# Kernel optimization log

Measured on AMD Instinct MI355X. Metric: run time of the kernel, lower is better.

The kernel has to match this reference:

```python
import jax, jax.numpy as jnp
import numpy as np


def setup_inputs() -> dict:
    key = jax.random.key(0)
    k1, k2 = jax.random.split(key)
    B, L, D = 8, 2048, 256
    x = jax.random.normal(k1, (B, L, D), dtype=jnp.float32)
    x_mask = jax.random.randint(k2, (B, L), 0, 2).astype(bool)  # True = padded key position
    return {"x": x, "x_mask": x_mask}


def reference(x, x_mask):
    # x: [B, L, D], x_mask: [B, L] bool (True = masked/padding)
    B, L, D = x.shape
    # Unscaled self-attention scores: [B, L, L]
    scores = jnp.einsum('bld,bmd->blm', x, x)
    # Diagonal exclusion: score of token with itself set to 0 (not -inf!)
    eye = jnp.eye(L, dtype=bool)
    scores = jnp.where(eye[None, :, :], jnp.float32(0.0), scores)
    # Padding mask: mask key columns with -inf (applied after diagonal zeroing,
    # so a masked diagonal entry ends up -inf, matching the torch order of ops)
    scores = jnp.where(x_mask[:, None, :], -jnp.inf, scores)
    a = jax.nn.softmax(scores, axis=2)
    return jnp.einsum('blm,bmd->bld', a, x)
```

## Files before the change

kernel.cpp:

```cpp
#include <hip/hip_runtime.h>
#include <hip/hip_bf16.h>

#define B_ 8
#define L_ 2048
#define D_ 256
#define BK 32
#define KSPLIT 2
#define KQ (L_/KSPLIT)
#define NIT (KQ/BK)
#define PSTR 40
#define NROW (B_*L_)
#define NE ((size_t)B_*L_*D_)
#define THR 13.0f
#define MINIT (-1e30f)
#define LOG2E_F 1.44269504f

typedef __attribute__((ext_vector_type(8))) _Float16 f16x8;
typedef __attribute__((ext_vector_type(4))) _Float16 hf4;
typedef __attribute__((ext_vector_type(4))) float f32x4;

#define MFMA16F(a,b,c) __builtin_amdgcn_mfma_f32_16x16x32_f16((a),(b),(c),0,0,0)
#define NEG_INF (-__builtin_inff())
#define GLL(src,dst) __builtin_amdgcn_global_load_lds( \
    (const __attribute__((address_space(1))) void*)(src), \
    (__attribute__((address_space(3))) void*)(dst), 16, 0, 0)

__device__ __forceinline__ f32x4 fmax4(f32x4 a, f32x4 b){
  f32x4 r;
  r[0]=fmaxf(a[0],b[0]); r[1]=fmaxf(a[1],b[1]);
  r[2]=fmaxf(a[2],b[2]); r[3]=fmaxf(a[3],b[3]);
  return r;
}

__global__ void prep_k(const float* __restrict__ x,
                       _Float16* __restrict__ x16,
                       _Float16* __restrict__ vtl){
  __shared__ _Float16 T[32][258];
  const int t = threadIdx.x;
  const int tIdx = blockIdx.x;
  const int b = blockIdx.y;
  const int l0 = tIdx*32;

  #pragma unroll
  for (int i=0;i<4;++i){
    const int n8 = t + 256*i;
    const int row = n8>>5;
    const int c   = (n8&31)*8;
    size_t idx = ((size_t)(b*L_ + l0 + row))*D_ + c;
    float4 v0 = *(const float4*)(x + idx);
    float4 v1 = *(const float4*)(x + idx + 4);
    f16x8 h;
    h[0]=(_Float16)v0.x; h[1]=(_Float16)v0.y; h[2]=(_Float16)v0.z; h[3]=(_Float16)v0.w;
    h[4]=(_Float16)v1.x; h[5]=(_Float16)v1.y; h[6]=(_Float16)v1.z; h[7]=(_Float16)v1.w;
    *(f16x8*)(x16 + idx) = h;
    *(f16x8*)(&T[row][c]) = h;
  }
  __syncthreads();

  _Float16* vb = vtl + ((size_t)(b*64 + tIdx))*8192;
  #pragma unroll
  for (int i=0;i<4;++i){
    const int q = t + 256*i;
    const int d = q>>2, ph = q&3;
    const int kc = ph ^ ((d>>1)&3);
    const int k0 = kc*8;
    f16x8 h;
    #pragma unroll
    for (int j=0;j<8;++j) h[j] = T[k0+j][d];
    *(f16x8*)(vb + (size_t)q*8) = h;
  }
}

__launch_bounds__(256, 2)
__global__ void flash_k(const _Float16* __restrict__ x16,
                        const _Float16* __restrict__ vtl,
                        const int* __restrict__ mask,
                        _Float16* __restrict__ oall,
                        float* __restrict__ mll,
                        float* __restrict__ mm){
  __shared__ __attribute__((aligned(16))) _Float16 sK[2][8192];
  __shared__ __attribute__((aligned(16))) _Float16 sV[2][8192];
  __shared__ __attribute__((aligned(16))) _Float16 sP[2][4][16*PSTR];

  const int tid  = threadIdx.x;
  const int wave = tid >> 6, lane = tid & 63;
  const int quad = lane >> 4, l16 = lane & 15;
  const int b = blockIdx.y, z = blockIdx.z;
  const int q0w = blockIdx.x*64 + wave*16;
  const int sw = l16 & 7, vsw = (l16>>1)&3;

  f16x8 qh[8];
  {
    const _Float16* qr = x16 + ((size_t)(b*L_ + q0w + l16))*D_;
    const _Float16 l2e = (_Float16)LOG2E_F;
    #pragma unroll
    for (int ks=0; ks<8; ++ks){
      f16x8 h = *(const f16x8*)(qr + ks*32 + quad*8);
      #pragma unroll
      for (int j=0;j<8;++j) h[j] = h[j] * l2e;
      qh[ks] = h;
    }
  }
  unsigned long long mb = 0;
  {
    const int* mrow = mask + b*L_ + z*KQ;
    #pragma unroll
    for (int j=0;j<64;++j)
      mb |= (unsigned long long)(mrow[j*16 + l16] ? 1u : 0u) << j;
  }

  f32x4 M = (f32x4){MINIT, MINIT, MINIT, MINIT};

  unsigned kof[4], vof[4], dof[4];
  #pragma unroll
  for (int i=0;i<4;++i){
    int c = (wave + i*4)*64 + lane;
    int r = c>>5, pk = c&31;
    kof[i] = (unsigned)(r*512 + ((pk ^ (r&7))*16));
    vof[i] = (unsigned)(c*16);
    dof[i] = (unsigned)((wave + i*4)*1024);
  }
  const char* kbase = (const char*)x16 + ((size_t)b*L_ + (size_t)z*KQ)*(D_*2);
  const char* vbase = (const char*)vtl + ((size_t)(b*64 + z*32))*16384;

  #pragma unroll
  for (int i=0;i<4;++i) GLL(kbase + kof[i], (char*)sK[0] + dof[i]);

  f32x4 O[16], Osum;
  #pragma unroll
  for (int i=0;i<16;i++) O[i] = (f32x4){0.f,0.f,0.f,0.f};
  Osum = (f32x4){0.f,0.f,0.f,0.f};
  f16x8 ones;
  #pragma unroll
  for (int j=0;j<8;++j) ones[j] = (_Float16)1.0f;

  __syncthreads();

  for (int it=0; it<NIT; ++it){
    if (it+1 < NIT){
      const char* kb2 = kbase + (size_t)(it+1)*16384;
      char* kd = (char*)sK[(it+1)&1];
      #pragma unroll
      for (int i=0;i<4;++i) GLL(kb2 + kof[i], kd + dof[i]);
    }
    {
      const char* vb2 = vbase + (size_t)it*16384;
      char* vd = (char*)sV[it&1];
      #pragma unroll
      for (int i=0;i<4;++i) GLL(vb2 + vof[i], vd + dof[i]);
    }
    const _Float16* kb = sK[it&1];

    f32x4 S[2];
    S[0]=(f32x4){0,0,0,0}; S[1]=(f32x4){0,0,0,0};
    #pragma unroll
    for (int ks=0; ks<8; ++ks){
      f16x8 b0 = *(const f16x8*)(kb + (     l16)*256 + (((ks*4+quad)^sw)*8));
      f16x8 b1 = *(const f16x8*)(kb + (16 + l16)*256 + (((ks*4+quad)^sw)*8));
      S[0] = MFMA16F(qh[ks], b0, S[0]);
      S[1] = MFMA16F(qh[ks], b1, S[1]);
    }

    if (it > 0){
      const _Float16* vb = sV[(it-1)&1];
      f16x8 pf = *(const f16x8*)(&sP[(it-1)&1][wave][l16*PSTR + quad*8]);
      #pragma unroll
      for (int vt=0; vt<16; ++vt){
        f16x8 bv = *(const f16x8*)(vb + (vt*16+l16)*32 + ((quad^vsw)*8));
        O[vt] = MFMA16F(pf, bv, O[vt]);
      }
      Osum = MFMA16F(pf, ones, Osum);
    }

    {
      const int d0 = q0w - (z*KQ + it*BK);
      if ((unsigned)d0 < 32u){
        const int ntd = d0 >> 4;
        #pragma unroll
        for (int r=0;r<4;++r)
          S[ntd][r] = (l16 == quad*4+r) ? 0.0f : S[ntd][r];
      }
    }
    {
      const unsigned mw = (unsigned)(mb >> (unsigned)(it*2));
      const float mk0 = (mw & 1u) ? NEG_INF : 0.0f;
      const float mk1 = (mw & 2u) ? NEG_INF : 0.0f;
      #pragma unroll
      for (int r=0;r<4;++r){ S[0][r] += mk0; S[1][r] += mk1; }
    }

    {
      f32x4 t = fmax4(S[0], S[1]);
      int ok = 1;
      #pragma unroll
      for (int r=0;r<4;++r) ok &= (t[r] <= M[r] + THR);
      if (!__all(ok)){
        #pragma unroll
        for (int off=1; off<16; off<<=1){
          f32x4 o;
          o[0]=__shfl_xor(t[0],off); o[1]=__shfl_xor(t[1],off);
          o[2]=__shfl_xor(t[2],off); o[3]=__shfl_xor(t[3],off);
          t = fmax4(t,o);
        }
        f32x4 mn = fmax4(M, t);
        float sc[4];
        #pragma unroll
        for (int r=0;r<4;++r) sc[r] = exp2f(M[r] - mn[r]);
        #pragma unroll
        for (int vt=0; vt<16; ++vt){
          #pragma unroll
          for (int r=0;r<4;++r) O[vt][r] *= sc[r];
        }
        #pragma unroll
        for (int r=0;r<4;++r) Osum[r] *= sc[r];
        M = mn;
      }
    }

    #pragma unroll
    for (int r=0;r<4;++r){
      const int row = quad*4 + r;
      sP[it&1][wave][row*PSTR +      l16] = (_Float16)exp2f(S[0][r] - M[r]);
      sP[it&1][wave][row*PSTR + 16 + l16] = (_Float16)exp2f(S[1][r] - M[r]);
    }

    __syncthreads();
  }

  {
    const _Float16* vb = sV[(NIT-1)&1];
    f16x8 pf = *(const f16x8*)(&sP[(NIT-1)&1][wave][l16*PSTR + quad*8]);
    #pragma unroll
    for (int vt=0; vt<16; ++vt){
      f16x8 bv = *(const f16x8*)(vb + (vt*16+l16)*32 + ((quad^vsw)*8));
      O[vt] = MFMA16F(pf, bv, O[vt]);
    }
    Osum = MFMA16F(pf, ones, Osum);
  }

  {
    const int u = b*(L_/16) + blockIdx.x*4 + wave;
    _Float16* ob = oall + (size_t)z*NE + (size_t)u*4096;
    #pragma unroll
    for (int vt=0; vt<16; ++vt){
      hf4 hh;
      #pragma unroll
      for (int r=0;r<4;++r) hh[r] = (_Float16)O[vt][r];
      *(hf4*)(ob + vt*256 + lane*4) = hh;
    }
    if (l16 == 0){
      const int row = u*16 + quad*4;
      #pragma unroll
      for (int r=0;r<4;++r){
        mll[z*NROW + row + r] = Osum[r];
        mm [z*NROW + row + r] = M[r];
      }
    }
  }
}

__global__ void combine_k(float* __restrict__ out,
                          const _Float16* __restrict__ oall,
                          const float* __restrict__ mll,
                          const float* __restrict__ mm){
  __shared__ float T2[16][260];
  const int t = threadIdx.x, u = blockIdx.x;
  const int quad = (t>>4)&3, l16 = t&15;
  const int row0 = u*16 + quad*4;

  f32x4 mz[KSPLIT], lz[KSPLIT];
  #pragma unroll
  for (int zc=0; zc<KSPLIT; ++zc){
    mz[zc] = *(const f32x4*)(mm  + zc*NROW + row0);
    lz[zc] = *(const f32x4*)(mll + zc*NROW + row0);
  }
  f32x4 ms = mz[0];
  #pragma unroll
  for (int zc=1; zc<KSPLIT; ++zc) ms = fmax4(ms, mz[zc]);

  float sc[KSPLIT][4];
  f32x4 den = (f32x4){0.f,0.f,0.f,0.f};
  #pragma unroll
  for (int zc=0; zc<KSPLIT; ++zc){
    #pragma unroll
    for (int r=0;r<4;++r){
      sc[zc][r] = exp2f(mz[zc][r] - ms[r]);
      den[r] += sc[zc][r] * lz[zc][r];
    }
  }
  float inv[4];
  #pragma unroll
  for (int r=0;r<4;++r) inv[r] = 1.0f/den[r];

  #pragma unroll
  for (int i=0;i<4;++i){
    const int f = t + 256*i;
    const int vt = f>>6;
    float acc[4] = {0.f,0.f,0.f,0.f};
    #pragma unroll
    for (int zc=0; zc<KSPLIT; ++zc){
      hf4 v = *(const hf4*)(oall + (size_t)zc*NE + (size_t)u*4096 + (size_t)f*4);
      #pragma unroll
      for (int r=0;r<4;++r) acc[r] += sc[zc][r] * (float)v[r];
    }
    #pragma unroll
    for (int r=0;r<4;++r) T2[quad*4+r][vt*16+l16] = acc[r]*inv[r];
  }
  __syncthreads();
  #pragma unroll
  for (int p=0;p<4;++p){
    const int row = (t>>6) + p*4, col = (t&63)*4;
    float4 vv = *(const float4*)&T2[row][col];
    *(float4*)(out + ((size_t)u*16 + row)*D_ + col) = vv;
  }
}

extern "C" void kernel_launch(void* const* d_in, const int* in_sizes, int n_in,
                              void* d_out, int out_size, void* d_ws, size_t ws_size,
                              hipStream_t stream) {
  const float* x    = (const float*)d_in[0];
  const int*   mask = (const int*)d_in[1];
  float*       out  = (float*)d_out;

  _Float16* x16  = (_Float16*)d_ws;
  _Float16* vtl  = x16 + NE;
  _Float16* oall = vtl + NE;
  float*    mll  = (float*)(oall + (size_t)KSPLIT*NE);
  float*    mm   = mll + (size_t)KSPLIT*NROW;

  prep_k   <<<dim3(L_/32, B_), dim3(256), 0, stream>>>(x, x16, vtl);
  flash_k  <<<dim3(L_/64, B_, KSPLIT), dim3(256), 0, stream>>>(x16, vtl, mask, oall, mll, mm);
  combine_k<<<dim3(NROW/16), dim3(256), 0, stream>>>(out, oall, mll, mm);
}
```

Baseline: 148.4 us.

## Fuse prep, flash and combine into one cooperative kernel with grid syncs

Replaces the three launches with a single cooperative kernel of 512 blocks. Each block first does the fp16 conversion and V transpose, then runs a grid sync, then the split-K flash pass. After a second grid sync, the z=0 blocks merge the z=1 partial results straight from their registers. This removes two kernel launch gaps and the z=0 half of the partial-output round trip through global memory. In exchange it pays for two grid-wide barriers, and it needs all 512 blocks resident at two per CU, with a fallback to the old three-kernel path if the cooperative launch fails.

```diff
diff --git a/kernel.cpp b/kernel.cpp
--- a/kernel.cpp
+++ b/kernel.cpp
@@ -1,5 +1,7 @@
 #include <hip/hip_runtime.h>
-#include <hip/hip_bf16.h>
+#include <hip/hip_cooperative_groups.h>
+
+namespace cg = cooperative_groups;
 
 #define B_ 8
 #define L_ 2048
@@ -32,21 +34,18 @@
   return r;
 }
 
-__global__ void prep_k(const float* __restrict__ x,
-                       _Float16* __restrict__ x16,
-                       _Float16* __restrict__ vtl){
-  __shared__ _Float16 T[32][258];
-  const int t = threadIdx.x;
-  const int tIdx = blockIdx.x;
-  const int b = blockIdx.y;
+__device__ __forceinline__ void prep_core(const float* __restrict__ x,
+                                          _Float16* __restrict__ x16,
+                                          _Float16* __restrict__ vtl,
+                                          int tIdx, int bb, int t, char* smem){
+  _Float16 (*T)[258] = (_Float16(*)[258])smem;
   const int l0 = tIdx*32;
-
   #pragma unroll
   for (int i=0;i<4;++i){
     const int n8 = t + 256*i;
     const int row = n8>>5;
     const int c   = (n8&31)*8;
-    size_t idx = ((size_t)(b*L_ + l0 + row))*D_ + c;
+    size_t idx = ((size_t)(bb*L_ + l0 + row))*D_ + c;
     float4 v0 = *(const float4*)(x + idx);
     float4 v1 = *(const float4*)(x + idx + 4);
     f16x8 h;
@@ -56,8 +55,7 @@
     *(f16x8*)(&T[row][c]) = h;
   }
   __syncthreads();
-
-  _Float16* vb = vtl + ((size_t)(b*64 + tIdx))*8192;
+  _Float16* vb = vtl + ((size_t)(bb*64 + tIdx))*8192;
   #pragma unroll
   for (int i=0;i<4;++i){
     const int q = t + 256*i;
@@ -71,22 +69,19 @@
   }
 }
 
-__launch_bounds__(256, 2)
-__global__ void flash_k(const _Float16* __restrict__ x16,
-                        const _Float16* __restrict__ vtl,
-                        const int* __restrict__ mask,
-                        _Float16* __restrict__ oall,
-                        float* __restrict__ mll,
-                        float* __restrict__ mm){
-  __shared__ __attribute__((aligned(16))) _Float16 sK[2][8192];
-  __shared__ __attribute__((aligned(16))) _Float16 sV[2][8192];
-  __shared__ __attribute__((aligned(16))) _Float16 sP[2][4][16*PSTR];
-
-  const int tid  = threadIdx.x;
-  const int wave = tid >> 6, lane = tid & 63;
+__device__ __forceinline__ void flash_core(const _Float16* __restrict__ x16,
+                                           const _Float16* __restrict__ vtl,
+                                           const int* __restrict__ mask,
+                                           char* smem, int b, int z, int qblk,
+                                           int wave, int lane,
+                                           f32x4 (&O)[16], f32x4& Osum, f32x4& M){
+  _Float16 (*sK)[8192] = (_Float16(*)[8192])smem;
+  _Float16 (*sV)[8192] = (_Float16(*)[8192])(smem + 32768);
+  typedef _Float16 sPhalf[4][16*PSTR];
+  sPhalf* sP = (sPhalf*)(smem + 65536);
+
   const int quad = lane >> 4, l16 = lane & 15;
-  const int b = blockIdx.y, z = blockIdx.z;
-  const int q0w = blockIdx.x*64 + wave*16;
+  const int q0w = qblk*64 + wave*16;
   const int sw = l16 & 7, vsw = (l16>>1)&3;
 
   f16x8 qh[8];
@@ -109,7 +104,7 @@
       mb |= (unsigned long long)(mrow[j*16 + l16] ? 1u : 0u) << j;
   }
 
-  f32x4 M = (f32x4){MINIT, MINIT, MINIT, MINIT};
+  M = (f32x4){MINIT, MINIT, MINIT, MINIT};
 
   unsigned kof[4], vof[4], dof[4];
   #pragma unroll
@@ -126,7 +121,6 @@
   #pragma unroll
   for (int i=0;i<4;++i) GLL(kbase + kof[i], (char*)sK[0] + dof[i]);
 
-  f32x4 O[16], Osum;
   #pragma unroll
   for (int i=0;i<16;i++) O[i] = (f32x4){0.f,0.f,0.f,0.f};
   Osum = (f32x4){0.f,0.f,0.f,0.f};
@@ -237,10 +231,34 @@
     }
     Osum = MFMA16F(pf, ones, Osum);
   }
-
-  {
-    const int u = b*(L_/16) + blockIdx.x*4 + wave;
-    _Float16* ob = oall + (size_t)z*NE + (size_t)u*4096;
+}
+
+__launch_bounds__(256, 2)
+__global__ void fused_k(const float* __restrict__ x,
+                        const int* __restrict__ mask,
+                        float* __restrict__ out,
+                        _Float16* __restrict__ x16,
+                        _Float16* __restrict__ vtl,
+                        _Float16* __restrict__ oall,
+                        float* __restrict__ mll,
+                        float* __restrict__ mm){
+  __shared__ __attribute__((aligned(16))) char smem[75776];
+  const int tid = threadIdx.x;
+  const int bid = blockIdx.x;
+  const int wave = tid >> 6, lane = tid & 63;
+  const int quad = lane >> 4, l16 = lane & 15;
+
+  prep_core(x, x16, vtl, bid & 63, bid >> 6, tid, smem);
+  cg::this_grid().sync();
+
+  const int z = bid >> 8, b = (bid >> 5) & 7, qblk = bid & 31;
+  f32x4 O[16], Osum, M;
+  flash_core(x16, vtl, mask, smem, b, z, qblk, wave, lane, O, Osum, M);
+
+  const int u = b*(L_/16) + qblk*4 + wave;
+
+  if (z == 1){
+    _Float16* ob = oall + (size_t)u*4096;
     #pragma unroll
     for (int vt=0; vt<16; ++vt){
       hf4 hh;
@@ -252,17 +270,87 @@
       const int row = u*16 + quad*4;
       #pragma unroll
       for (int r=0;r<4;++r){
-        mll[z*NROW + row + r] = Osum[r];
-        mm [z*NROW + row + r] = M[r];
+        mll[row + r] = Osum[r];
+        mm [row + r] = M[r];
       }
     }
   }
-}
-
-__global__ void combine_k(float* __restrict__ out,
-                          const _Float16* __restrict__ oall,
-                          const float* __restrict__ mll,
-                          const float* __restrict__ mm){
+  cg::this_grid().sync();
+  if (z == 1) return;
+
+  const int row0 = u*16 + quad*4;
+  f32x4 mz1 = *(const f32x4*)(mm  + row0);
+  f32x4 lz1 = *(const f32x4*)(mll + row0);
+  f32x4 ms = fmax4(M, mz1);
+  float s0[4], s1[4], inv[4];
+  #pragma unroll
+  for (int r=0;r<4;++r){
+    s0[r] = exp2f(M[r]   - ms[r]);
+    s1[r] = exp2f(mz1[r] - ms[r]);
+    inv[r] = 1.0f/(s0[r]*Osum[r] + s1[r]*lz1[r]);
+  }
+
+  float* t2 = (float*)smem + wave*4160;
+  #pragma unroll
+  for (int vt=0; vt<16; ++vt){
+    hf4 v1 = *(const hf4*)(oall + (size_t)u*4096 + vt*256 + lane*4);
+    #pragma unroll
+    for (int r=0;r<4;++r)
+      t2[(quad*4+r)*260 + vt*16 + l16] =
+        (s0[r]*O[vt][r] + s1[r]*(float)v1[r]) * inv[r];
+  }
+  __syncthreads();
+  #pragma unroll
+  for (int p=0;p<16;++p){
+    float4 vv = *(const float4*)(t2 + p*260 + lane*4);
+    *(float4*)(out + ((size_t)(u*16 + p))*D_ + lane*4) = vv;
+  }
+}
+
+__global__ void prep_fb(const float* __restrict__ x,
+                        _Float16* __restrict__ x16,
+                        _Float16* __restrict__ vtl){
+  __shared__ __attribute__((aligned(16))) char smem[16512];
+  prep_core(x, x16, vtl, blockIdx.x, blockIdx.y, threadIdx.x, smem);
+}
+
+__launch_bounds__(256, 2)
+__global__ void flash_fb(const _Float16* __restrict__ x16,
+                         const _Float16* __restrict__ vtl,
+                         const int* __restrict__ mask,
+                         _Float16* __restrict__ oall,
+                         float* __restrict__ mll,
+                         float* __restrict__ mm){
+  __shared__ __attribute__((aligned(16))) char smem[75776];
+  const int tid = threadIdx.x;
+  const int wave = tid >> 6, lane = tid & 63;
+  const int quad = lane >> 4, l16 = lane & 15;
+  const int b = blockIdx.y, z = blockIdx.z;
+  f32x4 O[16], Osum, M;
+  flash_core(x16, vtl, mask, smem, b, z, blockIdx.x, wave, lane, O, Osum, M);
+  const int u = b*(L_/16) + blockIdx.x*4 + wave;
+  _Float16* ob = oall + (size_t)z*NE + (size_t)u*4096;
+  #pragma unroll
+  for (int vt=0; vt<16; ++vt){
+    hf4 hh;
+    #pragma unroll
+    for (int r=0;r<4;++r) hh[r] = (_Float16)O[vt][r];
+    *(hf4*)(ob + vt*256 + lane*4) = hh;
+  }
+  if (l16 == 0){
+    const int row = u*16 + quad*4;
+    #pragma unroll
+    for (int r=0;r<4;++r){
+      mll[z*NROW + row + r] = Osum[r];
+      mm [z*NROW + row + r] = M[r];
+    }
+  }
+}
+
+__global__ void combine_fb(float* __restrict__ out,
+                           const _Float16* __restrict__ oall,
+                           const float* __restrict__ mll,
+                           const float* __restrict__ mm){
   __shared__ float T2[16][260];
   const int t = threadIdx.x, u = blockIdx.x;
   const int quad = (t>>4)&3, l16 = t&15;
@@ -274,10 +362,7 @@
     mz[zc] = *(const f32x4*)(mm  + zc*NROW + row0);
     lz[zc] = *(const f32x4*)(mll + zc*NROW + row0);
   }
-  f32x4 ms = mz[0];
-  #pragma unroll
-  for (int zc=1; zc<KSPLIT; ++zc) ms = fmax4(ms, mz[zc]);
-
+  f32x4 ms = fmax4(mz[0], mz[1]);
   float sc[KSPLIT][4];
   f32x4 den = (f32x4){0.f,0.f,0.f,0.f};
   #pragma unroll
@@ -328,7 +413,15 @@
   float*    mll  = (float*)(oall + (size_t)KSPLIT*NE);
   float*    mm   = mll + (size_t)KSPLIT*NROW;
 
-  prep_k   <<<dim3(L_/32, B_), dim3(256), 0, stream>>>(x, x16, vtl);
-  flash_k  <<<dim3(L_/64, B_, KSPLIT), dim3(256), 0, stream>>>(x16, vtl, mask, oall, mll, mm);
-  combine_k<<<dim3(NROW/16), dim3(256), 0, stream>>>(out, oall, mll, mm);
-}
+  void* args[] = {(void*)&x, (void*)&mask, (void*)&out,
+                  (void*)&x16, (void*)&vtl, (void*)&oall,
+                  (void*)&mll, (void*)&mm};
+  hipError_t e = hipLaunchCooperativeKernel((const void*)fused_k,
+                                            dim3(512), dim3(256),
+                                            args, 0, stream);
+  if (e != hipSuccess){
+    prep_fb   <<<dim3(L_/32, B_),        dim3(256), 0, stream>>>(x, x16, vtl);
+    flash_fb  <<<dim3(L_/64, B_, KSPLIT),dim3(256), 0, stream>>>(x16, vtl, mask, oall, mll, mm);
+    combine_fb<<<dim3(NROW/16),          dim3(256), 0, stream>>>(out, oall, mll, mm);
+  }
+}
```

New measurement: 258.6 us. +74.2%, slower.

## Split PV accumulation across wave pairs to halve V fragment LDS reads

Applied to the files above, without the earlier changes.

Waves are paired so that each wave computes the PV product for half of the D columns but for both waves' 16 query rows, reusing each loaded V fragment for two MFMAs. This halves per-wave V loads from LDS. The cost is that rescale factors must now cross waves: each wave publishes a flag and per-row scale factors through shared memory, and the partner wave applies them to the accumulator rows it holds for that wave's queries. Extra LDS traffic and branches are added for that exchange.

```diff
diff --git a/kernel.cpp b/kernel.cpp
--- a/kernel.cpp
+++ b/kernel.cpp
@@ -81,6 +81,8 @@
   __shared__ __attribute__((aligned(16))) _Float16 sK[2][8192];
   __shared__ __attribute__((aligned(16))) _Float16 sV[2][8192];
   __shared__ __attribute__((aligned(16))) _Float16 sP[2][4][16*PSTR];
+  __shared__ int   sFl[2][4];
+  __shared__ float sSc[2][4][16];
 
   const int tid  = threadIdx.x;
   const int wave = tid >> 6, lane = tid & 63;
@@ -88,6 +90,9 @@
   const int b = blockIdx.y, z = blockIdx.z;
   const int q0w = blockIdx.x*64 + wave*16;
   const int sw = l16 & 7, vsw = (l16>>1)&3;
+  const int p  = wave & 1;
+  const int ga = wave & 2;
+  const int og = ga + (p^1);
 
   f16x8 qh[8];
   {
@@ -162,14 +167,27 @@
     }
 
     if (it > 0){
+      if (sFl[(it-1)&1][og]){
+        f32x4 bs;
+        #pragma unroll
+        for (int r=0;r<4;++r) bs[r] = sSc[(it-1)&1][og][quad*4+r];
+        #pragma unroll
+        for (int lvt=0; lvt<8; ++lvt){
+          const int oi = p ? lvt : 8+lvt;
+          #pragma unroll
+          for (int r=0;r<4;++r) O[oi][r] *= bs[r];
+        }
+      }
       const _Float16* vb = sV[(it-1)&1];
-      f16x8 pf = *(const f16x8*)(&sP[(it-1)&1][wave][l16*PSTR + quad*8]);
-      #pragma unroll
-      for (int vt=0; vt<16; ++vt){
-        f16x8 bv = *(const f16x8*)(vb + (vt*16+l16)*32 + ((quad^vsw)*8));
-        O[vt] = MFMA16F(pf, bv, O[vt]);
-      }
-      Osum = MFMA16F(pf, ones, Osum);
+      f16x8 pf0 = *(const f16x8*)(&sP[(it-1)&1][ga  ][l16*PSTR + quad*8]);
+      f16x8 pf1 = *(const f16x8*)(&sP[(it-1)&1][ga+1][l16*PSTR + quad*8]);
+      #pragma unroll
+      for (int lvt=0; lvt<8; ++lvt){
+        f16x8 bv = *(const f16x8*)(vb + (((p*8+lvt)*16)+l16)*32 + ((quad^vsw)*8));
+        O[lvt]   = MFMA16F(pf0, bv, O[lvt]);
+        O[8+lvt] = MFMA16F(pf1, bv, O[8+lvt]);
+      }
+      Osum = MFMA16F(p ? pf1 : pf0, ones, Osum);
     }
 
     {
@@ -207,13 +225,21 @@
         #pragma unroll
         for (int r=0;r<4;++r) sc[r] = exp2f(M[r] - mn[r]);
         #pragma unroll
-        for (int vt=0; vt<16; ++vt){
+        for (int lvt=0; lvt<8; ++lvt){
+          const int oi = p ? 8+lvt : lvt;
           #pragma unroll
-          for (int r=0;r<4;++r) O[vt][r] *= sc[r];
+          for (int r=0;r<4;++r) O[oi][r] *= sc[r];
         }
         #pragma unroll
         for (int r=0;r<4;++r) Osum[r] *= sc[r];
         M = mn;
+        if (l16 == 0){
+          #pragma unroll
+          for (int r=0;r<4;++r) sSc[it&1][wave][quad*4+r] = sc[r];
+        }
+        if (lane == 0) sFl[it&1][wave] = 1;
+      } else {
+        if (lane == 0) sFl[it&1][wave] = 0;
       }
     }
 
@@ -228,28 +254,43 @@
   }
 
   {
+    if (sFl[(NIT-1)&1][og]){
+      f32x4 bs;
+      #pragma unroll
+      for (int r=0;r<4;++r) bs[r] = sSc[(NIT-1)&1][og][quad*4+r];
+      #pragma unroll
+      for (int lvt=0; lvt<8; ++lvt){
+        const int oi = p ? lvt : 8+lvt;
+        #pragma unroll
+        for (int r=0;r<4;++r) O[oi][r] *= bs[r];
+      }
+    }
     const _Float16* vb = sV[(NIT-1)&1];
-    f16x8 pf = *(const f16x8*)(&sP[(NIT-1)&1][wave][l16*PSTR + quad*8]);
-    #pragma unroll
-    for (int vt=0; vt<16; ++vt){
-      f16x8 bv = *(const f16x8*)(vb + (vt*16+l16)*32 + ((quad^vsw)*8));
-      O[vt] = MFMA16F(pf, bv, O[vt]);
-    }
-    Osum = MFMA16F(pf, ones, Osum);
+    f16x8 pf0 = *(const f16x8*)(&sP[(NIT-1)&1][ga  ][l16*PSTR + quad*8]);
+    f16x8 pf1 = *(const f16x8*)(&sP[(NIT-1)&1][ga+1][l16*PSTR + quad*8]);
+    #pragma unroll
+    for (int lvt=0; lvt<8; ++lvt){
+      f16x8 bv = *(const f16x8*)(vb + (((p*8+lvt)*16)+l16)*32 + ((quad^vsw)*8));
+      O[lvt]   = MFMA16F(pf0, bv, O[lvt]);
+      O[8+lvt] = MFMA16F(pf1, bv, O[8+lvt]);
+    }
+    Osum = MFMA16F(p ? pf1 : pf0, ones, Osum);
   }
 
   {
-    const int u = b*(L_/16) + blockIdx.x*4 + wave;
-    _Float16* ob = oall + (size_t)z*NE + (size_t)u*4096;
-    #pragma unroll
-    for (int vt=0; vt<16; ++vt){
-      hf4 hh;
-      #pragma unroll
-      for (int r=0;r<4;++r) hh[r] = (_Float16)O[vt][r];
-      *(hf4*)(ob + vt*256 + lane*4) = hh;
+    const int ub = b*(L_/16) + blockIdx.x*4;
+    _Float16* ob0 = oall + (size_t)z*NE + (size_t)(ub+ga  )*4096;
+    _Float16* ob1 = oall + (size_t)z*NE + (size_t)(ub+ga+1)*4096;
+    #pragma unroll
+    for (int lvt=0; lvt<8; ++lvt){
+      hf4 h0, h1;
+      #pragma unroll
+      for (int r=0;r<4;++r){ h0[r] = (_Float16)O[lvt][r]; h1[r] = (_Float16)O[8+lvt][r]; }
+      *(hf4*)(ob0 + (p*8+lvt)*256 + lane*4) = h0;
+      *(hf4*)(ob1 + (p*8+lvt)*256 + lane*4) = h1;
     }
     if (l16 == 0){
-      const int row = u*16 + quad*4;
+      const int row = (ub + wave)*16 + quad*4;
       #pragma unroll
       for (int r=0;r<4;++r){
         mll[z*NROW + row + r] = Osum[r];
```

Result: slower. 433.7 us (+192.2%).
